# Optimization experiments

Hardware: AMD Instinct MI355X
Metric: run time of the kernel (lower is better)

The kernel has to match this reference:

```python
import jax, jax.numpy as jnp
import numpy as np

B, S = 4, 2048          # batch, seq tokens
D_IN, D_HID = 1280, 2048  # from CAMERAMOE emb_size / d_inner
E, K = 8, 2             # num_experts, top_k
LN_EPS = 1e-6


def setup_inputs() -> dict:
    key = jax.random.key(0)
    ks = jax.random.split(key, 8)
    rn = lambda k, shp, sc=1.0: jax.random.normal(k, shp, dtype=jnp.float32) * sc
    return {
        "x": rn(ks[0], (B, S, D_IN)),
        "noise": rn(ks[1], (B, S, E)),          # the randn_like draw, made explicit
        "wr": rn(ks[2], (D_IN, E), 0.02), "br": jnp.zeros((E,), jnp.float32),
        "wn": rn(ks[3], (D_IN, E), 0.02), "bn": jnp.zeros((E,), jnp.float32),
        "w1": rn(ks[4], (E, D_IN, D_HID), 0.02), "b1": jnp.zeros((E, D_HID), jnp.float32),
        "w2": rn(ks[5], (E, D_HID, D_IN), 0.02), "b2": jnp.zeros((E, D_IN), jnp.float32),
        "gamma": jnp.ones((E, D_IN), jnp.float32), "beta": jnp.zeros((E, D_IN), jnp.float32),
    }


def reference(x, noise, wr, br, wn, bn, w1, b1, w2, b2, gamma, beta):
    # --- NoisyTopkRouter ---
    logits = x @ wr + br                                  # [B,S,E]
    noise_logits = x @ wn + bn                            # [B,S,E]
    noisy = logits + noise * jax.nn.softplus(noise_logits)
    _, idx = jax.lax.top_k(noisy, K)                      # [B,S,K]
    sel = jax.nn.one_hot(idx, E, dtype=bool).any(axis=-2) # [B,S,E] selected-expert mask
    sparse_logits = jnp.where(sel, noisy, -jnp.inf)       # scatter of top-k logits into -inf
    gates = jax.nn.softmax(sparse_logits, axis=-1)        # zeros for non-selected experts

    # --- SparseMoE combine (gate-weighted sum over experts; gate==0 masks out
    # non-selected tokens, matching the torch masked gather/scatter-add math) ---
    h = jax.nn.relu(jnp.einsum('bsd,edh->ebsh', x, w1) + b1[:, None, None, :])
    y = jnp.einsum('ebsh,ehd->ebsd', h, w2) + b2[:, None, None, :]
    y = y + x                                             # residual (broadcast over E)
    mu = y.mean(axis=-1, keepdims=True)
    var = y.var(axis=-1, keepdims=True)
    y = (y - mu) * jax.lax.rsqrt(var + LN_EPS)
    y = y * gamma[:, None, None, :] + beta[:, None, None, :]
    return jnp.einsum('ebsd,bse->bsd', y, gates)          # [B,S,D_IN]
```

## Files before the change

### kernel.cpp

```cpp
#include <hip/hip_runtime.h>
#include <stdint.h>

typedef unsigned short u16;
typedef __attribute__((ext_vector_type(8))) short short8;
typedef __attribute__((ext_vector_type(4))) float f32x4;
typedef __attribute__((ext_vector_type(4))) float float4v;
typedef __attribute__((ext_vector_type(4))) unsigned short us4;

#define TOK   8192
#define DIN   1280
#define DHID  2048
#define NEXP  8
#define RCAP  17408
#define MT128 136

__device__ __forceinline__ float bf2f(u16 u) {
  union { unsigned int i; float f; } v; v.i = ((unsigned int)u) << 16; return v.f;
}
__device__ __forceinline__ u16 f2bf(float f) {
  union { float f; unsigned int i; } v; v.f = f;
  unsigned int x = v.i;
  return (u16)((x + 0x7fffu + ((x >> 16) & 1u)) >> 16);
}

__device__ __forceinline__ void gload16(const u16* g, void* lds) {
  __builtin_amdgcn_global_load_lds(
      (const __attribute__((address_space(1))) unsigned int*)g,
      (__attribute__((address_space(3))) unsigned int*)lds, 16, 0, 0);
}

__global__ __launch_bounds__(256) void router_k(
    const float* __restrict__ x, const float* __restrict__ noise,
    const float* __restrict__ wr, const float* __restrict__ br,
    const float* __restrict__ wn, const float* __restrict__ bn,
    int* __restrict__ topk_e, float* __restrict__ topk_g)
{
  int w = threadIdx.x >> 6, lane = threadIdx.x & 63;
  int t0 = blockIdx.x * 8 + w * 2;
  const float4v* xA = (const float4v*)(x + (size_t)t0 * DIN);
  const float4v* xB = (const float4v*)(x + (size_t)(t0 + 1) * DIN);
  float accA[16], accB[16];
  #pragma unroll
  for (int k = 0; k < 16; k++) { accA[k] = 0.f; accB[k] = 0.f; }

  #pragma unroll
  for (int i = 0; i < 5; i++) {
    int d4 = i * 64 + lane;
    float4v va = xA[d4];
    float4v vb = xB[d4];
    #pragma unroll
    for (int j = 0; j < 4; j++) {
      int d = d4 * 4 + j;
      const float4v* wrp = (const float4v*)(wr + (size_t)d * 8);
      const float4v* wnp = (const float4v*)(wn + (size_t)d * 8);
      float4v r0 = wrp[0], r1 = wrp[1], n0 = wnp[0], n1 = wnp[1];
      float a = va[j], b = vb[j];
      #pragma unroll
      for (int e = 0; e < 4; e++) {
        accA[e]    += a * r0[e]; accA[e+4]  += a * r1[e];
        accA[e+8]  += a * n0[e]; accA[e+12] += a * n1[e];
        accB[e]    += b * r0[e]; accB[e+4]  += b * r1[e];
        accB[e+8]  += b * n0[e]; accB[e+12] += b * n1[e];
      }
    }
  }
  #pragma unroll
  for (int k = 0; k < 16; k++) {
    float v = accA[k];
    for (int off = 32; off; off >>= 1) v += __shfl_xor(v, off);
    accA[k] = v;
    float u = accB[k];
    for (int off = 32; off; off >>= 1) u += __shfl_xor(u, off);
    accB[k] = u;
  }
  if (lane == 0) {
    #pragma unroll
    for (int tt = 0; tt < 2; tt++) {
      int t = t0 + tt;
      float noisy[8];
      #pragma unroll
      for (int e = 0; e < 8; e++) {
        float lg = (tt ? accB[e] : accA[e]) + br[e];
        float nl = (tt ? accB[e+8] : accA[e+8]) + bn[e];
        float sp = (nl > 0.f) ? nl + log1pf(expf(-nl)) : log1pf(expf(nl));
        noisy[e] = lg + noise[(size_t)t * 8 + e] * sp;
      }
      int e0 = 0; float v0 = noisy[0];
      #pragma unroll
      for (int e = 1; e < 8; e++) if (noisy[e] > v0) { v0 = noisy[e]; e0 = e; }
      int e1 = -1; float v1 = -1e30f;
      #pragma unroll
      for (int e = 0; e < 8; e++) if (e != e0 && noisy[e] > v1) { v1 = noisy[e]; e1 = e; }
      float g0 = 1.f / (1.f + expf(v1 - v0));
      topk_e[2*t] = e0; topk_e[2*t+1] = e1;
      topk_g[2*t] = g0; topk_g[2*t+1] = 1.f - g0;
    }
  }
}

__global__ __launch_bounds__(1024) void scan_k(
    const int* __restrict__ topk_e, int* __restrict__ rowmap, int* __restrict__ aoffs)
{
  __shared__ int cnt[1024][8];
  __shared__ int tot[8];
  __shared__ int base[8];
  int tid = threadIdx.x;
  int ebuf[16];
  #pragma unroll
  for (int j = 0; j < 16; j++) ebuf[j] = topk_e[tid * 16 + j];
  int c0=0,c1=0,c2=0,c3=0,c4=0,c5=0,c6=0,c7=0;
  #pragma unroll
  for (int j = 0; j < 16; j++) {
    int e = ebuf[j];
    c0 += (e==0); c1 += (e==1); c2 += (e==2); c3 += (e==3);
    c4 += (e==4); c5 += (e==5); c6 += (e==6); c7 += (e==7);
  }
  cnt[tid][0]=c0; cnt[tid][1]=c1; cnt[tid][2]=c2; cnt[tid][3]=c3;
  cnt[tid][4]=c4; cnt[tid][5]=c5; cnt[tid][6]=c6; cnt[tid][7]=c7;
  __syncthreads();

  int w = tid >> 6, lane = tid & 63;
  if (w < 8) {
    int e = w;
    int s[16]; int run = 0;
    #pragma unroll
    for (int j = 0; j < 16; j++) { s[j] = run; run += cnt[lane*16+j][e]; }
    int inc = run;
    for (int off = 1; off < 64; off <<= 1) {
      int v = __shfl_up(inc, off);
      if (lane >= off) inc += v;
    }
    int lane_excl = inc - run;
    #pragma unroll
    for (int j = 0; j < 16; j++) cnt[lane*16+j][e] = lane_excl + s[j];
    if (lane == 63) tot[e] = inc;
  }
  __syncthreads();
  if (tid == 0) {
    int a = 0;
    for (int e = 0; e < 8; e++) { base[e] = a; aoffs[e] = a; a += (tot[e] + 127) & ~127; }
    aoffs[8] = a;
  }
  __syncthreads();
  int o0 = base[0]+cnt[tid][0], o1 = base[1]+cnt[tid][1], o2 = base[2]+cnt[tid][2],
      o3 = base[3]+cnt[tid][3], o4 = base[4]+cnt[tid][4], o5 = base[5]+cnt[tid][5],
      o6 = base[6]+cnt[tid][6], o7 = base[7]+cnt[tid][7];
  #pragma unroll
  for (int j = 0; j < 16; j++) {
    int e = ebuf[j];
    int row = o0;
    row = (e==1) ? o1 : row; row = (e==2) ? o2 : row; row = (e==3) ? o3 : row;
    row = (e==4) ? o4 : row; row = (e==5) ? o5 : row; row = (e==6) ? o6 : row;
    row = (e==7) ? o7 : row;
    o0 += (e==0); o1 += (e==1); o2 += (e==2); o3 += (e==3);
    o4 += (e==4); o5 += (e==5); o6 += (e==6); o7 += (e==7);
    rowmap[tid * 16 + j] = row;
  }
}

__global__ __launch_bounds__(256) void gather_k(
    const float* __restrict__ x, const int* __restrict__ rowmap,
    u16* __restrict__ Xe)
{
  int w = threadIdx.x >> 6, lane = threadIdx.x & 63;
  int p = blockIdx.x * 4 + w;
  int t = p >> 1;
  int row = rowmap[p];
  const float4v* xs = (const float4v*)(x + (size_t)t * DIN);
  us4* xd = (us4*)(Xe + (size_t)row * DIN);
  #pragma unroll
  for (int i = 0; i < DIN / 4 / 64; i++) {
    int q = i * 64 + lane;
    float4v v = xs[q];
    us4 o;
    #pragma unroll
    for (int j = 0; j < 4; j++) o[j] = f2bf(v[j]);
    xd[q] = o;
  }
}

__global__ __launch_bounds__(256) void transpose_k(
    const float* __restrict__ in, u16* __restrict__ out, int RK, int CN)
{
  __shared__ float tile[32][33];
  int e = blockIdx.z;
  const float* ine = in + (size_t)e * RK * CN;
  u16* oute = out + (size_t)e * RK * CN;
  int cb = blockIdx.x * 32, rb = blockIdx.y * 32;
  int c = threadIdx.x & 31, r4 = threadIdx.x >> 5;
  #pragma unroll
  for (int i = 0; i < 4; i++) {
    int r = r4 + i * 8;
    tile[r][c] = ine[(size_t)(rb + r) * CN + cb + c];
  }
  __syncthreads();
  #pragma unroll
  for (int i = 0; i < 4; i++) {
    int r = r4 + i * 8;
    oute[(size_t)(cb + r) * RK + rb + c] = f2bf(tile[c][r]);
  }
}

__global__ __launch_bounds__(256, 2) void gemm128_k(
    const u16* __restrict__ A, const u16* __restrict__ Bt,
    const float* __restrict__ bias, u16* __restrict__ Out,
    const int* __restrict__ aoffs, int K, int N, int relu)
{
  extern __shared__ u16 sm[];

  int nwgx = gridDim.x;
  int id = blockIdx.y * nwgx + blockIdx.x;
  int per = (nwgx * gridDim.y) >> 3;
  int sid = (id & 7) * per + (id >> 3);
  int bx = sid % nwgx, by = sid / nwgx;

  int row0 = by * 128;
  if (row0 >= aoffs[NEXP]) return;
  int e = 0;
  #pragma unroll
  for (int i = 0; i < NEXP; i++) if (row0 >= aoffs[i + 1]) e = i + 1;
  int ncol0 = bx * 128;
  const u16* Ab = A + (size_t)row0 * K;
  const u16* Bb = Bt + ((size_t)e * N + ncol0) * K;

  int tid = threadIdx.x, w = tid >> 6, lane = tid & 63;
  int wr = w >> 1, wc = w & 1;
  int l15 = lane & 15, l4 = lane >> 4;
  int xorv = (l15 & 7) << 3;

  int srow[4], skc[4];
  #pragma unroll
  for (int q = 0; q < 4; q++) {
    int cd = q * 256 + tid;
    int cs = cd ^ ((cd >> 3) & 7);
    srow[q] = cs >> 3;
    skc[q]  = (cs & 7) * 8;
  }
  int ldsw = w * 1024;

  f32x4 acc[4][4];
  #pragma unroll
  for (int m = 0; m < 4; m++)
    #pragma unroll
    for (int n = 0; n < 4; n++) acc[m][n] = (f32x4){0.f, 0.f, 0.f, 0.f};

  short8 a[4][2], b[2][2];

#define STAGE_A(T, BUF) do {                                                  \
    char* d_ = (char*)sm + (BUF) * 32768;                                     \
    int ko_ = (T) * 64;                                                       \
    _Pragma("unroll")                                                         \
    for (int q = 0; q < 4; q++)                                               \
      gload16(Ab + (size_t)srow[q] * K + ko_ + skc[q], d_ + q*4096 + ldsw);   \
  } while (0)
#define STAGE_B(T, BUF) do {                                                  \
    char* d_ = (char*)sm + (BUF) * 32768 + 16384;                             \
    int ko_ = (T) * 64;                                                       \
    _Pragma("unroll")                                                         \
    for (int q = 0; q < 4; q++)                                               \
      gload16(Bb + (size_t)srow[q] * K + ko_ + skc[q], d_ + q*4096 + ldsw);   \
  } while (0)
#define RD_A() do {                                                           \
    _Pragma("unroll")                                                         \
    for (int m = 0; m < 4; m++)                                               \
      _Pragma("unroll")                                                       \
      for (int ks = 0; ks < 2; ks++) {                                        \
        int r_ = wr*64 + m*16 + l15;                                          \
        a[m][ks] = *(const short8*)&smA[(r_*64 + ks*32 + l4*8) ^ xorv];       \
      }                                                                       \
  } while (0)
#define RD_B(NH) do {                                                         \
    _Pragma("unroll")                                                         \
    for (int n = 0; n < 2; n++)                                               \
      _Pragma("unroll")                                                       \
      for (int ks = 0; ks < 2; ks++) {                                        \
        int r_ = wc*64 + (NH)*32 + n*16 + l15;                                \
        b[n][ks] = *(const short8*)&smB[(r_*64 + ks*32 + l4*8) ^ xorv];       \
      }                                                                       \
  } while (0)
#define MFMA16(NH) do {                                                       \
    __builtin_amdgcn_s_setprio(1);                                            \
    _Pragma("unroll")                                                         \
    for (int m = 0; m < 4; m++)                                               \
      _Pragma("unroll")                                                       \
      for (int n = 0; n < 2; n++)                                             \
        _Pragma("unroll")                                                     \
        for (int ks = 0; ks < 2; ks++)                                        \
          acc[m][(NH)*2+n] = __builtin_amdgcn_mfma_f32_16x16x32_bf16(         \
              a[m][ks], b[n][ks], acc[m][(NH)*2+n], 0, 0, 0);                 \
    __builtin_amdgcn_s_setprio(0);                                            \
  } while (0)
#define BAR __builtin_amdgcn_s_barrier()

  int NT = K >> 6;
  STAGE_A(0, 0);
  STAGE_B(0, 0);
  STAGE_A(1, 1);
  asm volatile("s_waitcnt vmcnt(4)" ::: "memory");
  BAR;

  for (int t = 0; t < NT; ++t) {
    int buf = t & 1;
    const u16* smA = sm + buf * 16384;
    const u16* smB = smA + 8192;
    RD_A();
    RD_B(0);
    if (t + 1 < NT) STAGE_B(t + 1, buf ^ 1);
    BAR;
    MFMA16(0);
    BAR;
    RD_B(1);
    if (t + 2 < NT) STAGE_A(t + 2, buf);
    BAR;
    MFMA16(1);
    if (t + 2 < NT) {
      asm volatile("s_waitcnt vmcnt(4)" ::: "memory");
    } else if (t + 1 < NT) {
      asm volatile("s_waitcnt vmcnt(0)" ::: "memory");
    }
    BAR;
  }
#undef STAGE_A
#undef STAGE_B
#undef RD_A
#undef RD_B
#undef MFMA16
#undef BAR

  #pragma unroll
  for (int in = 0; in < 4; in++) {
    int c = ncol0 + wc * 64 + in * 16 + l15;
    float bv = bias[(size_t)e * N + c];
    #pragma unroll
    for (int im = 0; im < 4; im++) {
      int rb = row0 + wr * 64 + im * 16 + l4 * 4;
      #pragma unroll
      for (int j = 0; j < 4; j++) {
        float v = acc[im][in][j] + bv;
        if (relu) v = fmaxf(v, 0.f);
        Out[(size_t)(rb + j) * N + c] = f2bf(v);
      }
    }
  }
}

__global__ __launch_bounds__(256) void ln_k(
    const float* __restrict__ x, const u16* __restrict__ Y,
    const int* __restrict__ rowmap, const int* __restrict__ topk_e,
    const float* __restrict__ topk_g, const float* __restrict__ gamma,
    const float* __restrict__ beta, float* __restrict__ out)
{
  __shared__ float red[4][4];
  int t = blockIdx.x, tid = threadIdx.x;
  int r0 = rowmap[2*t], r1 = rowmap[2*t+1];
  int e0 = topk_e[2*t], e1 = topk_e[2*t+1];
  float g0 = topk_g[2*t], g1 = topk_g[2*t+1];
  const float* xt = x + (size_t)t * DIN;
  const u16* y0p = Y + (size_t)r0 * DIN;
  const u16* y1p = Y + (size_t)r1 * DIN;
  float v0[5], v1[5];
  float s0 = 0.f, q0 = 0.f, s1 = 0.f, q1 = 0.f;
  #pragma unroll
  for (int i = 0; i < 5; i++) {
    int d = i * 256 + tid;
    float xv = xt[d];
    float a = xv + bf2f(y0p[d]);
    float b = xv + bf2f(y1p[d]);
    v0[i] = a; v1[i] = b;
    s0 += a; q0 += a * a; s1 += b; q1 += b * b;
  }
  for (int off = 32; off; off >>= 1) {
    s0 += __shfl_xor(s0, off); q0 += __shfl_xor(q0, off);
    s1 += __shfl_xor(s1, off); q1 += __shfl_xor(q1, off);
  }
  int w = tid >> 6, lane = tid & 63;
  if (lane == 0) { red[w][0] = s0; red[w][1] = q0; red[w][2] = s1; red[w][3] = q1; }
  __syncthreads();
  s0 = red[0][0] + red[1][0] + red[2][0] + red[3][0];
  q0 = red[0][1] + red[1][1] + red[2][1] + red[3][1];
  s1 = red[0][2] + red[1][2] + red[2][2] + red[3][2];
  q1 = red[0][3] + red[1][3] + red[2][3] + red[3][3];
  const float inv = 1.f / DIN;
  float mu0 = s0 * inv, mu1 = s1 * inv;
  float rs0 = rsqrtf(fmaxf(q0 * inv - mu0 * mu0, 0.f) + 1e-6f);
  float rs1 = rsqrtf(fmaxf(q1 * inv - mu1 * mu1, 0.f) + 1e-6f);
  const float* ga0 = gamma + (size_t)e0 * DIN;
  const float* be0 = beta  + (size_t)e0 * DIN;
  const float* ga1 = gamma + (size_t)e1 * DIN;
  const float* be1 = beta  + (size_t)e1 * DIN;
  #pragma unroll
  for (int i = 0; i < 5; i++) {
    int d = i * 256 + tid;
    float n0 = (v0[i] - mu0) * rs0 * ga0[d] + be0[d];
    float n1 = (v1[i] - mu1) * rs1 * ga1[d] + be1[d];
    out[(size_t)t * DIN + d] = g0 * n0 + g1 * n1;
  }
}

extern "C" void kernel_launch(void* const* d_in, const int* in_sizes, int n_in,
                              void* d_out, int out_size, void* d_ws, size_t ws_size,
                              hipStream_t stream)
{
  const float* x     = (const float*)d_in[0];
  const float* noise = (const float*)d_in[1];
  const float* wr    = (const float*)d_in[2];
  const float* br    = (const float*)d_in[3];
  const float* wn    = (const float*)d_in[4];
  const float* bn    = (const float*)d_in[5];
  const float* w1    = (const float*)d_in[6];
  const float* b1    = (const float*)d_in[7];
  const float* w2    = (const float*)d_in[8];
  const float* b2    = (const float*)d_in[9];
  const float* gamma = (const float*)d_in[10];
  const float* beta  = (const float*)d_in[11];
  float* out = (float*)d_out;
  char* ws = (char*)d_ws;

  int*   aoffs   = (int*)(ws + 128);
  int*   rowmap  = (int*)(ws + 4096);
  int*   topk_e  = (int*)(ws + 4096 + 65536);
  float* topk_g  = (float*)(ws + 4096 + 2 * 65536);

  const size_t XE_OFF   = (size_t)1 << 20;
  const size_t XE_BYTES = (size_t)RCAP * DIN * 2;
  const size_t H_BYTES  = (size_t)RCAP * DHID * 2;
  const size_t WT_BYTES = (size_t)NEXP * DHID * DIN * 2;
  u16* Xe  = (u16*)(ws + XE_OFF);
  u16* Hb  = (u16*)(ws + XE_OFF + XE_BYTES);
  u16* Yb  = Xe;
  u16* W1t = (u16*)(ws + XE_OFF + XE_BYTES + H_BYTES);
  u16* W2t = (u16*)(ws + XE_OFF + XE_BYTES + H_BYTES + WT_BYTES);

  transpose_k<<<dim3(DHID/32, DIN/32, NEXP), 256, 0, stream>>>(w1, W1t, DIN, DHID);
  transpose_k<<<dim3(DIN/32, DHID/32, NEXP), 256, 0, stream>>>(w2, W2t, DHID, DIN);
  router_k<<<TOK/8, 256, 0, stream>>>(x, noise, wr, br, wn, bn, topk_e, topk_g);
  scan_k<<<1, 1024, 0, stream>>>(topk_e, rowmap, aoffs);
  gather_k<<<TOK*2/4, 256, 0, stream>>>(x, rowmap, Xe);
  gemm128_k<<<dim3(DHID/128, MT128), 256, 65536, stream>>>(Xe, W1t, b1, Hb, aoffs, DIN, DHID, 1);
  gemm128_k<<<dim3(DIN/128, MT128), 256, 65536, stream>>>(Hb, W2t, b2, Yb, aoffs, DHID, DIN, 0);
  ln_k<<<TOK, 256, 0, stream>>>(x, Yb, rowmap, topk_e, topk_g, gamma, beta, out);
}
```

Measured before the change: 371.5 us.

## Fuse transposes with router and deepen GEMM prefetch with fewer barriers

Merges both weight transpose kernels and the router into one launch to cut launch gaps and let the independent work overlap. Restructures the GEMM main loop so A and B tiles are prefetched two iterations ahead, both B halves are read up front, and barriers per k-step drop from four to two. This uses more registers (two B fragment sets) and changes how much load latency is hidden.

```diff
diff --git a/kernel.cpp b/kernel.cpp
--- a/kernel.cpp
+++ b/kernel.cpp
@@ -14,6 +14,10 @@
 #define RCAP  17408
 #define MT128 136
 
+#define T1BLKS 20480
+#define T2BLKS 20480
+#define RTRBLKS 1024
+
 __device__ __forceinline__ float bf2f(u16 u) {
   union { unsigned int i; float f; } v; v.i = ((unsigned int)u) << 16; return v.f;
 }
@@ -29,14 +33,49 @@
       (__attribute__((address_space(3))) unsigned int*)lds, 16, 0, 0);
 }
 
-__global__ __launch_bounds__(256) void router_k(
+__global__ __launch_bounds__(256) void pre_k(
+    const float* __restrict__ w1, u16* __restrict__ W1t,
+    const float* __restrict__ w2, u16* __restrict__ W2t,
     const float* __restrict__ x, const float* __restrict__ noise,
     const float* __restrict__ wr, const float* __restrict__ br,
     const float* __restrict__ wn, const float* __restrict__ bn,
     int* __restrict__ topk_e, float* __restrict__ topk_g)
 {
+  __shared__ float tile[32][33];
+  int id = blockIdx.x;
+
+  if (id < T1BLKS + T2BLKS) {
+    const float* in; u16* out; int RK, CN, cb, rb, e;
+    if (id < T1BLKS) {
+      e = id / 2560; int r = id % 2560;
+      RK = DIN; CN = DHID;
+      cb = (r & 63) * 32; rb = (r >> 6) * 32;
+      in = w1 + (size_t)e * RK * CN; out = W1t + (size_t)e * RK * CN;
+    } else {
+      int id2 = id - T1BLKS;
+      e = id2 / 2560; int r = id2 % 2560;
+      RK = DHID; CN = DIN;
+      cb = (r % 40) * 32; rb = (r / 40) * 32;
+      in = w2 + (size_t)e * RK * CN; out = W2t + (size_t)e * RK * CN;
+    }
+    int c = threadIdx.x & 31, r4 = threadIdx.x >> 5;
+    #pragma unroll
+    for (int i = 0; i < 4; i++) {
+      int r = r4 + i * 8;
+      tile[r][c] = in[(size_t)(rb + r) * CN + cb + c];
+    }
+    __syncthreads();
+    #pragma unroll
+    for (int i = 0; i < 4; i++) {
+      int r = r4 + i * 8;
+      out[(size_t)(cb + r) * RK + rb + c] = f2bf(tile[c][r]);
+    }
+    return;
+  }
+
+  int rid = id - (T1BLKS + T2BLKS);
   int w = threadIdx.x >> 6, lane = threadIdx.x & 63;
-  int t0 = blockIdx.x * 8 + w * 2;
+  int t0 = rid * 8 + w * 2;
   const float4v* xA = (const float4v*)(x + (size_t)t0 * DIN);
   const float4v* xB = (const float4v*)(x + (size_t)(t0 + 1) * DIN);
   float accA[16], accB[16];
@@ -179,28 +218,6 @@
   }
 }
 
-__global__ __launch_bounds__(256) void transpose_k(
-    const float* __restrict__ in, u16* __restrict__ out, int RK, int CN)
-{
-  __shared__ float tile[32][33];
-  int e = blockIdx.z;
-  const float* ine = in + (size_t)e * RK * CN;
-  u16* oute = out + (size_t)e * RK * CN;
-  int cb = blockIdx.x * 32, rb = blockIdx.y * 32;
-  int c = threadIdx.x & 31, r4 = threadIdx.x >> 5;
-  #pragma unroll
-  for (int i = 0; i < 4; i++) {
-    int r = r4 + i * 8;
-    tile[r][c] = ine[(size_t)(rb + r) * CN + cb + c];
-  }
-  __syncthreads();
-  #pragma unroll
-  for (int i = 0; i < 4; i++) {
-    int r = r4 + i * 8;
-    oute[(size_t)(cb + r) * RK + rb + c] = f2bf(tile[c][r]);
-  }
-}
-
 __global__ __launch_bounds__(256, 2) void gemm128_k(
     const u16* __restrict__ A, const u16* __restrict__ Bt,
     const float* __restrict__ bias, u16* __restrict__ Out,
@@ -244,7 +261,7 @@
     #pragma unroll
     for (int n = 0; n < 4; n++) acc[m][n] = (f32x4){0.f, 0.f, 0.f, 0.f};
 
-  short8 a[4][2], b[2][2];
+  short8 a[4][2], b0[2][2], b1[2][2];
 
 #define STAGE_A(T, BUF) do {                                                  \
     char* d_ = (char*)sm + (BUF) * 32768;                                     \
@@ -269,17 +286,16 @@
         a[m][ks] = *(const short8*)&smA[(r_*64 + ks*32 + l4*8) ^ xorv];       \
       }                                                                       \
   } while (0)
-#define RD_B(NH) do {                                                         \
+#define RD_B(DST, NH) do {                                                    \
     _Pragma("unroll")                                                         \
     for (int n = 0; n < 2; n++)                                               \
       _Pragma("unroll")                                                       \
       for (int ks = 0; ks < 2; ks++) {                                        \
         int r_ = wc*64 + (NH)*32 + n*16 + l15;                                \
-        b[n][ks] = *(const short8*)&smB[(r_*64 + ks*32 + l4*8) ^ xorv];       \
+        DST[n][ks] = *(const short8*)&smB[(r_*64 + ks*32 + l4*8) ^ xorv];     \
       }                                                                       \
   } while (0)
-#define MFMA16(NH) do {                                                       \
-    __builtin_amdgcn_s_setprio(1);                                            \
+#define MFMA16(NH, BB) do {                                                   \
     _Pragma("unroll")                                                         \
     for (int m = 0; m < 4; m++)                                               \
       _Pragma("unroll")                                                       \
@@ -287,8 +303,7 @@
         _Pragma("unroll")                                                     \
         for (int ks = 0; ks < 2; ks++)                                        \
           acc[m][(NH)*2+n] = __builtin_amdgcn_mfma_f32_16x16x32_bf16(         \
-              a[m][ks], b[n][ks], acc[m][(NH)*2+n], 0, 0, 0);                 \
-    __builtin_amdgcn_s_setprio(0);                                            \
+              a[m][ks], BB[n][ks], acc[m][(NH)*2+n], 0, 0, 0);                \
   } while (0)
 #define BAR __builtin_amdgcn_s_barrier()
 
@@ -296,7 +311,8 @@
   STAGE_A(0, 0);
   STAGE_B(0, 0);
   STAGE_A(1, 1);
-  asm volatile("s_waitcnt vmcnt(4)" ::: "memory");
+  STAGE_B(1, 1);
+  asm volatile("s_waitcnt vmcnt(8)" ::: "memory");
   BAR;
 
   for (int t = 0; t < NT; ++t) {
@@ -304,17 +320,20 @@
     const u16* smA = sm + buf * 16384;
     const u16* smB = smA + 8192;
     RD_A();
-    RD_B(0);
-    if (t + 1 < NT) STAGE_B(t + 1, buf ^ 1);
+    RD_B(b0, 0);
+    RD_B(b1, 1);
+    asm volatile("s_waitcnt lgkmcnt(0)" ::: "memory");
     BAR;
-    MFMA16(0);
-    BAR;
-    RD_B(1);
-    if (t + 2 < NT) STAGE_A(t + 2, buf);
-    BAR;
-    MFMA16(1);
     if (t + 2 < NT) {
-      asm volatile("s_waitcnt vmcnt(4)" ::: "memory");
+      STAGE_A(t + 2, buf);
+      STAGE_B(t + 2, buf);
+    }
+    __builtin_amdgcn_s_setprio(1);
+    MFMA16(0, b0);
+    MFMA16(1, b1);
+    __builtin_amdgcn_s_setprio(0);
+    if (t + 2 < NT) {
+      asm volatile("s_waitcnt vmcnt(8)" ::: "memory");
     } else if (t + 1 < NT) {
       asm volatile("s_waitcnt vmcnt(0)" ::: "memory");
     }
@@ -431,9 +450,8 @@
   u16* W1t = (u16*)(ws + XE_OFF + XE_BYTES + H_BYTES);
   u16* W2t = (u16*)(ws + XE_OFF + XE_BYTES + H_BYTES + WT_BYTES);
 
-  transpose_k<<<dim3(DHID/32, DIN/32, NEXP), 256, 0, stream>>>(w1, W1t, DIN, DHID);
-  transpose_k<<<dim3(DIN/32, DHID/32, NEXP), 256, 0, stream>>>(w2, W2t, DHID, DIN);
-  router_k<<<TOK/8, 256, 0, stream>>>(x, noise, wr, br, wn, bn, topk_e, topk_g);
+  pre_k<<<T1BLKS + T2BLKS + RTRBLKS, 256, 0, stream>>>(
+      w1, W1t, w2, W2t, x, noise, wr, br, wn, bn, topk_e, topk_g);
   scan_k<<<1, 1024, 0, stream>>>(topk_e, rowmap, aoffs);
   gather_k<<<TOK*2/4, 256, 0, stream>>>(x, rowmap, Xe);
   gemm128_k<<<dim3(DHID/128, MT128), 256, 65536, stream>>>(Xe, W1t, b1, Hb, aoffs, DIN, DHID, 1);
```

After: 361.6 us. 1.03x faster.
